# Kernel optimization log

Measured on AMD Instinct MI355X. Metric: run time of the kernel, lower is better.

Reference implementation:

```python
import jax, jax.numpy as jnp
import numpy as np

NOISE_DIM = 128
IN_FEATURES = 512
OUT_FEATURES = 512
BATCH = 256


def setup_inputs() -> dict:
    key = jax.random.key(0)
    k1, k2, k3 = jax.random.split(key, 3)
    out_dim = IN_FEATURES * OUT_FEATURES + OUT_FEATURES
    # x = [noise | features]
    x = jax.random.normal(k1, (BATCH, NOISE_DIM + IN_FEATURES), dtype=jnp.float32)
    # hypermodel Linear params; scale ~ 1/sqrt(fan_in) like torch default init
    scale = 1.0 / np.sqrt(NOISE_DIM)
    W = jax.random.uniform(k2, (NOISE_DIM, out_dim), dtype=jnp.float32, minval=-scale, maxval=scale)
    b = jax.random.uniform(k3, (out_dim,), dtype=jnp.float32, minval=-scale, maxval=scale)
    return {"x": x, "W": W, "b": b}


def reference(x, W, b):
    # split input into hypernet noise and features
    noise = x[:, :NOISE_DIM]            # [B, noise_dim]
    feats = x[:, NOISE_DIM:]            # [B, in_features]
    # hypermodel: generate per-sample linear params
    params = noise @ W + b              # [B, in*out + out]
    w_flat = params[:, : IN_FEATURES * OUT_FEATURES]
    bias = params[:, IN_FEATURES * OUT_FEATURES :]        # [B, out]
    weight = w_flat.reshape(-1, IN_FEATURES, OUT_FEATURES)  # [B, in, out]
    # batched matmul (torch.bmm of [B,1,in] @ [B,in,out]) + bias, squeeze
    out = jnp.einsum("bi,bio->bo", feats, weight) + bias   # [B, out]
    return out
```

## Files before the change

kernel.cpp:

```cpp
#include <hip/hip_runtime.h>
#include <hip/hip_bf16.h>
#include <stdint.h>

namespace {
constexpr int kBatch = 256;
constexpr int kNoise = 128;
constexpr int kIn    = 512;
constexpr int kOut   = 512;
constexpr int kXCols = kNoise + kIn;
constexpr int kPCols = kIn * kOut + kOut;
constexpr int kOTile = 32;
constexpr int kITile = 16;
constexpr int kSplits = kIn / kITile;
constexpr int kWStride = 68;
constexpr int kFeatsStride = 260;
constexpr int kSlab = kBatch * kOut + 64;
}

typedef __bf16 bf16x8 __attribute__((ext_vector_type(8)));
typedef float  f32x4  __attribute__((ext_vector_type(4)));
typedef unsigned int u32x4 __attribute__((ext_vector_type(4)));

__device__ inline unsigned int pack_bf16x2(float lo, float hi) {
    unsigned int a = (unsigned int)__builtin_bit_cast(unsigned short, (__bf16)lo);
    unsigned int b = (unsigned int)__builtin_bit_cast(unsigned short, (__bf16)hi);
    return a | (b << 16);
}

__device__ inline void wg_barrier_lds() {
    __asm__ volatile("" ::: "memory");
    __builtin_amdgcn_s_waitcnt(0xC07F);
    __builtin_amdgcn_s_barrier();
    __asm__ volatile("" ::: "memory");
}

__global__ __launch_bounds__(512, 4)
void hyper_gemm_kernel(const float* __restrict__ x,
                       const float* __restrict__ W,
                       const float* __restrict__ bvec,
                       float* __restrict__ part)
{
    const int tid  = threadIdx.x;
    const int lane = tid & 63;
    const int wave = tid >> 6;
    const int q    = lane >> 4;
    const int l16  = lane & 15;

    const int o0 = blockIdx.x * kOTile;
    const int i0 = blockIdx.y * kITile;

    const int u  = tid >> 3;
    const int c4 = (tid & 7) * 4;

    __shared__ unsigned int wtile[2][kOTile * kWStride];
    __shared__ float feats_lds[kITile * kFeatsStride];
    __shared__ float bv_lds[(kITile + 1) * kOTile];

    const int nPass = (blockIdx.y == 0) ? (kITile + 1) : kITile;

    auto pass_cbase = [&](int p) -> size_t {
        return (p == kITile) ? (size_t)(kIn * kOut) : (size_t)(i0 + p) * kOut;
    };
    auto wrow = [&](int p) -> const float* {
        return W + (size_t)(2 * u) * kPCols + pass_cbase(p) + o0 + c4;
    };

    f32x4 pA0, pA1, pB0, pB1, pC0, pC1;
    { const float* wp = wrow(0); pA0 = *(const f32x4*)wp; pA1 = *(const f32x4*)(wp + kPCols); }
    { const float* wp = wrow(1); pB0 = *(const f32x4*)wp; pB1 = *(const f32x4*)(wp + kPCols); }
    { const float* wp = wrow(2); pC0 = *(const f32x4*)wp; pC1 = *(const f32x4*)(wp + kPCols); }

    for (int idx = tid; idx < (kITile + 1) * kOTile; idx += 512) {
        const int p = idx >> 5, c = idx & 31;
        const size_t cb = (p == kITile) ? (size_t)(kIn * kOut) : (size_t)(i0 + p) * kOut;
        bv_lds[idx] = bvec[cb + o0 + c];
    }

    {
        const int i    = tid & 15;
        const int brow = tid >> 4;
        #pragma unroll
        for (int rep = 0; rep < 8; ++rep) {
            const int b = brow + rep * 32;
            feats_lds[i * kFeatsStride + b] = x[b * kXCols + kNoise + i0 + i];
        }
    }

    bf16x8 afrag[2][4];
    #pragma unroll
    for (int rt = 0; rt < 2; ++rt) {
        const float* xr = x + (size_t)(wave * 32 + rt * 16 + l16) * kXCols;
        #pragma unroll
        for (int s = 0; s < 4; ++s) {
            const float* p = xr + s * 32 + q * 8;
            f32x4 u0 = *(const f32x4*)(p);
            f32x4 u1 = *(const f32x4*)(p + 4);
            bf16x8 a;
            a[0] = (__bf16)u0[0]; a[1] = (__bf16)u0[1];
            a[2] = (__bf16)u0[2]; a[3] = (__bf16)u0[3];
            a[4] = (__bf16)u1[0]; a[5] = (__bf16)u1[1];
            a[6] = (__bf16)u1[2]; a[7] = (__bf16)u1[3];
            afrag[rt][s] = a;
        }
    }

    float oacc[2][2][4];
    #pragma unroll
    for (int rt = 0; rt < 2; ++rt)
        #pragma unroll
        for (int nt = 0; nt < 2; ++nt)
            #pragma unroll
            for (int r = 0; r < 4; ++r) oacc[rt][nt][r] = 0.f;

    __syncthreads();

    for (int ip = 0; ip < nPass; ++ip) {
        unsigned int pk0 = pack_bf16x2(pA0[0], pA1[0]);
        unsigned int pk1 = pack_bf16x2(pA0[1], pA1[1]);
        unsigned int pk2 = pack_bf16x2(pA0[2], pA1[2]);
        unsigned int pk3 = pack_bf16x2(pA0[3], pA1[3]);

        unsigned int* wt = &wtile[ip & 1][0];
        wt[(c4 + 0) * kWStride + u] = pk0;
        wt[(c4 + 1) * kWStride + u] = pk1;
        wt[(c4 + 2) * kWStride + u] = pk2;
        wt[(c4 + 3) * kWStride + u] = pk3;

        pA0 = pB0; pA1 = pB1; pB0 = pC0; pB1 = pC1;
        if (ip + 3 < nPass) {
            const float* wp = wrow(ip + 3);
            pC0 = *(const f32x4*)wp; pC1 = *(const f32x4*)(wp + kPCols);
        }

        wg_barrier_lds();

        f32x4 acc[2][2];
        const f32x4 zero = {0.f, 0.f, 0.f, 0.f};
        acc[0][0] = zero; acc[0][1] = zero; acc[1][0] = zero; acc[1][1] = zero;

        #pragma unroll
        for (int s = 0; s < 4; ++s) {
            #pragma unroll
            for (int nt = 0; nt < 2; ++nt) {
                u32x4 raw = *(const u32x4*)&wt[(nt * 16 + l16) * kWStride + s * 16 + q * 4];
                bf16x8 bfrag = __builtin_bit_cast(bf16x8, raw);
                acc[0][nt] = __builtin_amdgcn_mfma_f32_16x16x32_bf16(
                    afrag[0][s], bfrag, acc[0][nt], 0, 0, 0);
                acc[1][nt] = __builtin_amdgcn_mfma_f32_16x16x32_bf16(
                    afrag[1][s], bfrag, acc[1][nt], 0, 0, 0);
            }
        }

        const float bv0 = bv_lds[ip * kOTile + l16];
        const float bv1 = bv_lds[ip * kOTile + 16 + l16];

        if (ip < kITile) {
            #pragma unroll
            for (int rt = 0; rt < 2; ++rt) {
                const f32x4 f4 = *(const f32x4*)&feats_lds[ip * kFeatsStride
                                        + wave * 32 + rt * 16 + q * 4];
                #pragma unroll
                for (int r = 0; r < 4; ++r) {
                    oacc[rt][0][r] += f4[r] * (acc[rt][0][r] + bv0);
                    oacc[rt][1][r] += f4[r] * (acc[rt][1][r] + bv1);
                }
            }
        } else {
            #pragma unroll
            for (int rt = 0; rt < 2; ++rt)
                #pragma unroll
                for (int r = 0; r < 4; ++r) {
                    oacc[rt][0][r] += acc[rt][0][r] + bv0;
                    oacc[rt][1][r] += acc[rt][1][r] + bv1;
                }
        }
    }

    float* pp = part + (size_t)blockIdx.y * kSlab;
    #pragma unroll
    for (int rt = 0; rt < 2; ++rt)
        #pragma unroll
        for (int nt = 0; nt < 2; ++nt) {
            const int o = o0 + nt * 16 + l16;
            #pragma unroll
            for (int r = 0; r < 4; ++r) {
                const int b = wave * 32 + rt * 16 + q * 4 + r;
                pp[(size_t)b * kOut + o] = oacc[rt][nt][r];
            }
        }
}

__global__ __launch_bounds__(128)
void reduce_kernel(const float* __restrict__ part, float* __restrict__ out)
{
    const size_t idx4 = ((size_t)blockIdx.x * 128 + threadIdx.x) * 4;
    f32x4 acc = *(const f32x4*)(part + idx4);
    #pragma unroll
    for (int s = 1; s < kSplits; ++s)
        acc += *(const f32x4*)(part + (size_t)s * kSlab + idx4);
    *(f32x4*)(out + idx4) = acc;
}

extern "C" void kernel_launch(void* const* d_in, const int* in_sizes, int n_in,
                              void* d_out, int out_size, void* d_ws, size_t ws_size,
                              hipStream_t stream) {
    const float* x  = (const float*)d_in[0];
    const float* W  = (const float*)d_in[1];
    const float* bv = (const float*)d_in[2];
    float* out  = (float*)d_out;
    float* part = (float*)d_ws;

    dim3 grid(kOut / kOTile, kSplits);
    hyper_gemm_kernel<<<grid, 512, 0, stream>>>(x, W, bv, part);

    const int n4 = kBatch * kOut / 4;
    reduce_kernel<<<n4 / 128, 128, 0, stream>>>(part, out);
}
```

Measured before the change: 213.0 us.

## Restructure W staging into single-barrier pipelined LDS stores with scalar loads

W loads change from two f32x4 rows per thread to eight scalar loads along the noise dimension per thread. Each thread then packs them into one 128-bit LDS store instead of four scattered 32-bit stores. The loop now stores the next pass's tile after the barrier, which removes the initial syncthreads and keeps one barrier per pass, with a four-deep register prefetch. The reduce kernel uses two independent accumulators to shorten the add dependency chain. Scalar global loads may coalesce less efficiently per instruction and raise register pressure.

```diff
diff --git a/kernel.cpp b/kernel.cpp
--- a/kernel.cpp
+++ b/kernel.cpp
@@ -49,8 +49,8 @@
     const int o0 = blockIdx.x * kOTile;
     const int i0 = blockIdx.y * kITile;
 
-    const int u  = tid >> 3;
-    const int c4 = (tid & 7) * 4;
+    const int sw = tid >> 5;
+    const int sc = tid & 31;
 
     __shared__ unsigned int wtile[2][kOTile * kWStride];
     __shared__ float feats_lds[kITile * kFeatsStride];
@@ -61,14 +61,18 @@
     auto pass_cbase = [&](int p) -> size_t {
         return (p == kITile) ? (size_t)(kIn * kOut) : (size_t)(i0 + p) * kOut;
     };
-    auto wrow = [&](int p) -> const float* {
-        return W + (size_t)(2 * u) * kPCols + pass_cbase(p) + o0 + c4;
+    const float* wbase = W + (size_t)(8 * sw) * kPCols + o0 + sc;
+    auto loadpass = [&](int p, float* r) {
+        const float* wp = wbase + pass_cbase(p);
+        #pragma unroll
+        for (int rr = 0; rr < 8; ++rr) r[rr] = wp[(size_t)rr * kPCols];
     };
 
-    f32x4 pA0, pA1, pB0, pB1, pC0, pC1;
-    { const float* wp = wrow(0); pA0 = *(const f32x4*)wp; pA1 = *(const f32x4*)(wp + kPCols); }
-    { const float* wp = wrow(1); pB0 = *(const f32x4*)wp; pB1 = *(const f32x4*)(wp + kPCols); }
-    { const float* wp = wrow(2); pC0 = *(const f32x4*)wp; pC1 = *(const f32x4*)(wp + kPCols); }
+    float r0[8], rA[8], rB[8], rC[8];
+    loadpass(0, r0);
+    loadpass(1, rA);
+    loadpass(2, rB);
+    loadpass(3, rC);
 
     for (int idx = tid; idx < (kITile + 1) * kOTile; idx += 512) {
         const int p = idx >> 5, c = idx & 31;
@@ -104,6 +108,13 @@
         }
     }
 
+    {
+        u32x4 pk;
+        #pragma unroll
+        for (int j = 0; j < 4; ++j) pk[j] = pack_bf16x2(r0[2 * j], r0[2 * j + 1]);
+        *(u32x4*)&wtile[0][sc * kWStride + 4 * sw] = pk;
+    }
+
     float oacc[2][2][4];
     #pragma unroll
     for (int rt = 0; rt < 2; ++rt)
@@ -112,28 +123,20 @@
             #pragma unroll
             for (int r = 0; r < 4; ++r) oacc[rt][nt][r] = 0.f;
 
-    __syncthreads();
-
     for (int ip = 0; ip < nPass; ++ip) {
-        unsigned int pk0 = pack_bf16x2(pA0[0], pA1[0]);
-        unsigned int pk1 = pack_bf16x2(pA0[1], pA1[1]);
-        unsigned int pk2 = pack_bf16x2(pA0[2], pA1[2]);
-        unsigned int pk3 = pack_bf16x2(pA0[3], pA1[3]);
-
-        unsigned int* wt = &wtile[ip & 1][0];
-        wt[(c4 + 0) * kWStride + u] = pk0;
-        wt[(c4 + 1) * kWStride + u] = pk1;
-        wt[(c4 + 2) * kWStride + u] = pk2;
-        wt[(c4 + 3) * kWStride + u] = pk3;
-
-        pA0 = pB0; pA1 = pB1; pB0 = pC0; pB1 = pC1;
-        if (ip + 3 < nPass) {
-            const float* wp = wrow(ip + 3);
-            pC0 = *(const f32x4*)wp; pC1 = *(const f32x4*)(wp + kPCols);
-        }
-
         wg_barrier_lds();
 
+        if (ip + 1 < nPass) {
+            u32x4 pk;
+            #pragma unroll
+            for (int j = 0; j < 4; ++j) pk[j] = pack_bf16x2(rA[2 * j], rA[2 * j + 1]);
+            *(u32x4*)&wtile[(ip + 1) & 1][sc * kWStride + 4 * sw] = pk;
+        }
+        #pragma unroll
+        for (int rr = 0; rr < 8; ++rr) { rA[rr] = rB[rr]; rB[rr] = rC[rr]; }
+        if (ip + 4 < nPass) loadpass(ip + 4, rC);
+
+        const unsigned int* wt = &wtile[ip & 1][0];
         f32x4 acc[2][2];
         const f32x4 zero = {0.f, 0.f, 0.f, 0.f};
         acc[0][0] = zero; acc[0][1] = zero; acc[1][0] = zero; acc[1][1] = zero;
@@ -194,11 +197,14 @@
 void reduce_kernel(const float* __restrict__ part, float* __restrict__ out)
 {
     const size_t idx4 = ((size_t)blockIdx.x * 128 + threadIdx.x) * 4;
-    f32x4 acc = *(const f32x4*)(part + idx4);
-    #pragma unroll
-    for (int s = 1; s < kSplits; ++s)
-        acc += *(const f32x4*)(part + (size_t)s * kSlab + idx4);
-    *(f32x4*)(out + idx4) = acc;
+    f32x4 a0 = {0.f, 0.f, 0.f, 0.f};
+    f32x4 a1 = {0.f, 0.f, 0.f, 0.f};
+    #pragma unroll
+    for (int s = 0; s < kSplits; s += 2) {
+        a0 += *(const f32x4*)(part + (size_t)s * kSlab + idx4);
+        a1 += *(const f32x4*)(part + (size_t)(s + 1) * kSlab + idx4);
+    }
+    *(f32x4*)(out + idx4) = a0 + a1;
 }
 
 extern "C" void kernel_launch(void* const* d_in, const int* in_sizes, int n_in,
```

New measurement: 213.7 us. About the same (+0.3%).
